# Optimization experiments

Hardware: AMD Instinct MI355X
Metric: run time of the kernel (lower is better)

Reference implementation:

```python
import jax, jax.numpy as jnp
import numpy as np

B, A, G = 16, 32, 512      # batch, atoms, g_feat_in
S, M = 1024, 8             # subset samples, peaks per subset
E, OH = 5, 20              # element types, thermometer size per element
FE = E * OH                # formula encoding = 100
D = 512                    # internal_d
NBINS = 512                # spect bins
EPS = 1e-4


def _ln(x, g, b):
    m = x.mean(-1, keepdims=True)
    v = jnp.mean((x - m) ** 2, -1, keepdims=True)
    return (x - m) * jax.lax.rsqrt(v + 1e-5) * g + b


def setup_inputs() -> dict:
    key = jax.random.key(0)
    ks = jax.random.split(key, 16)
    vert_feat_in = jax.random.normal(ks[0], (B, A, G), jnp.float32)
    vert_mask_in = jnp.ones((B, A), jnp.float32)
    elem = jax.random.randint(ks[1], (B, A), 0, E)
    vert_element_oh = jax.nn.one_hot(elem, E, dtype=jnp.float32)
    atom_subsets = jax.random.randint(ks[2], (B, S, A), 0, 2).astype(jnp.int32)
    atom_subsets_peaks_mass_idx = jax.random.randint(ks[3], (B, S, M), 0, NBINS).astype(jnp.int32)
    atom_subsets_peaks_intensity = jax.random.uniform(ks[4], (B, S, M), jnp.float32)

    def lin(k, o, i):
        s = 1.0 / np.sqrt(i)
        return jax.random.uniform(k, (o, i), jnp.float32, -s, s)

    return dict(
        vert_feat_in=vert_feat_in, vert_mask_in=vert_mask_in,
        vert_element_oh=vert_element_oh, atom_subsets=atom_subsets,
        atom_subsets_peaks_mass_idx=atom_subsets_peaks_mass_idx,
        atom_subsets_peaks_intensity=atom_subsets_peaks_intensity,
        ln_sub_g=jnp.ones((G,)), ln_sub_b=jnp.zeros((G,)),
        W_ih=lin(ks[5], 3 * G, FE), W_hh=lin(ks[6], 3 * G, G),
        b_ih=jnp.zeros((3 * G,)), b_hh=jnp.zeros((3 * G,)),
        ln_post_g=jnp.ones((G,)), ln_post_b=jnp.zeros((G,)),
        W1=lin(ks[7], D, G), b1=jnp.zeros((D,)),
        W2a=lin(ks[8], D, D), b2a=jnp.zeros((D,)),
        W2b=lin(ks[9], D, D), b2b=jnp.zeros((D,)),
        ln_pre_g=jnp.ones((D,)), ln_pre_b=jnp.zeros((D,)),
        W_s=lin(ks[10], 1, D), b_s=jnp.zeros((1,)),
    )


def reference(vert_feat_in, vert_mask_in, vert_element_oh, atom_subsets,
              atom_subsets_peaks_mass_idx, atom_subsets_peaks_intensity,
              ln_sub_g, ln_sub_b, W_ih, W_hh, b_ih, b_hh,
              ln_post_g, ln_post_b, W1, b1, W2a, b2a, W2b, b2b,
              ln_pre_g, ln_pre_b, W_s, b_s):
    subs_f = atom_subsets.astype(jnp.float32)
    masked_vert = vert_feat_in * vert_mask_in[:, :, None]          # B,A,G
    subs_masked = subs_f * vert_mask_in[:, None, :]                 # B,S,A
    # subset-weighted pooling of vertex features
    swv_sum = jnp.einsum('baf,bsa->bsf', masked_vert, subs_masked)  # B,S,G
    subset_size = subs_masked.sum(-1) + EPS                         # B,S
    swv_mean = swv_sum / subset_size[..., None]
    h = _ln(swv_mean, ln_sub_g, ln_sub_b)                           # B,S,G
    # formula counts -> thermometer (accumulating) one-hot; .byte() cast kills grads
    counts = jax.lax.stop_gradient(
        jnp.einsum('bae,bsa->bse', vert_element_oh, subs_f))        # B,S,E
    therm = (jnp.arange(OH, dtype=jnp.float32)[None, None, None, :] < counts[..., None])
    formulae = therm.astype(jnp.float32).reshape(counts.shape[0], counts.shape[1], FE)
    # GRUCell: input=formula encoding, hidden=subset_normed
    gi = jnp.einsum('bsf,gf->bsg', formulae, W_ih) + b_ih           # B,S,3G
    gh = jnp.einsum('bsh,gh->bsg', h, W_hh) + b_hh
    gi_r, gi_z, gi_n = jnp.split(gi, 3, axis=-1)
    gh_r, gh_z, gh_n = jnp.split(gh, 3, axis=-1)
    r = jax.nn.sigmoid(gi_r + gh_r)
    z = jax.nn.sigmoid(gi_z + gh_z)
    n = jnp.tanh(gi_n + r * gh_n)
    combined = (1.0 - z) * n + z * h                                # B,S,G
    x = _ln(combined, ln_post_g, ln_post_b)
    x = jax.nn.relu(jnp.einsum('bsg,dg->bsd', x, W1) + b1)
    x = jax.nn.relu(jnp.einsum('bsd,ed->bse', x, W2a) + b2a)
    x = jax.nn.relu(jnp.einsum('bsd,ed->bse', x, W2b) + b2b)
    x = _ln(x, ln_pre_g, ln_pre_b)
    scores = (jnp.einsum('bsd,od->bso', x, W_s) + b_s)[..., 0]      # B,S
    probs = jax.nn.softmax(scores, axis=-1)                         # B,S
    # sparse mass-matrix multiply: scatter subset probs into spectrum bins
    weighted = atom_subsets_peaks_intensity * probs[:, :, None]     # B,S,M
    bidx = jnp.arange(probs.shape[0])[:, None, None]
    spect_out = jnp.zeros((probs.shape[0], NBINS), probs.dtype)
    spect_out = spect_out.at[bidx, atom_subsets_peaks_mass_idx].add(weighted)
    return spect_out, probs
```

## Files before the change

kernel.cpp:

```cpp
#include <hip/hip_runtime.h>

#define NB 16
#define NA 32
#define NG 512
#define NS 1024
#define NM 8
#define NE 5
#define NOH 20
#define NFE 100
#define ND 512
#define NBINS 512
#define NTOK (NB * NS)

typedef unsigned short ushort_t;
typedef __attribute__((ext_vector_type(8))) short bf16x8;
typedef __attribute__((ext_vector_type(4))) float f32x4;

__device__ __forceinline__ ushort_t f2bf(float x) {
  union { float f; unsigned u; } v; v.f = x;
  unsigned r = v.u + 0x7FFF + ((v.u >> 16) & 1);
  return (ushort_t)(r >> 16);
}
__device__ __forceinline__ float bf2f(ushort_t b) {
  union { unsigned u; float f; } v; v.u = ((unsigned)b) << 16;
  return v.f;
}

__device__ __forceinline__ void gload_lds16(const void* g, void* l) {
  __builtin_amdgcn_global_load_lds(
      (const __attribute__((address_space(1))) void*)g,
      (__attribute__((address_space(3))) void*)l, 16, 0, 0);
}

__device__ __forceinline__ float wsum64(float v) {
#pragma unroll
  for (int off = 32; off > 0; off >>= 1) v += __shfl_xor(v, off);
  return v;
}

__device__ __forceinline__ float fsig(float x) {
  return __builtin_amdgcn_rcpf(1.f + __expf(-x));
}
__device__ __forceinline__ float ftanh(float x) {
  float t = fminf(fmaxf(x, -15.f), 15.f);
  return 1.f - 2.f * __builtin_amdgcn_rcpf(__expf(2.f * t) + 1.f);
}

__global__ __launch_bounds__(256) void setup_kernel(
    const float* __restrict__ vert, const float* __restrict__ mask,
    const float* __restrict__ eloh, const int* __restrict__ subs,
    const float* __restrict__ Wih, const float* __restrict__ bih,
    const float* __restrict__ Whh,
    const float* __restrict__ W1, const float* __restrict__ W2a,
    const float* __restrict__ W2b,
    float* __restrict__ tcd, ushort_t* __restrict__ PSb,
    ushort_t* __restrict__ o_hh, ushort_t* __restrict__ o1,
    ushort_t* __restrict__ o2a, ushort_t* __restrict__ o2b,
    ushort_t* __restrict__ VmT, ushort_t* __restrict__ S_bf) {
  int i = blockIdx.x * 256 + threadIdx.x;
  if (i < NTOK) {
    int b = i >> 10;
    const int* srow = subs + (size_t)i * NA;
    float cnt[NE] = {0.f, 0.f, 0.f, 0.f, 0.f};
    float z = 0.f;
    for (int a = 0; a < NA; a++) {
      float sb = (float)srow[a];
      z += sb * mask[b * NA + a];
      const float* eo = eloh + (size_t)(b * NA + a) * NE;
#pragma unroll
      for (int e = 0; e < NE; e++) cnt[e] += eo[e] * sb;
    }
    float* o = tcd + (size_t)i * 8;
#pragma unroll
    for (int e = 0; e < NE; e++) o[e] = cnt[e];
    o[5] = 1.0f / (z + 1e-4f);
    return;
  }
  i -= NTOK;
  if (i < NE * 1536) {
    int e = i / 1536, g = i % 1536;
    float s = (e == 0) ? bih[g] : 0.f;
    ushort_t* base = PSb + ((size_t)e * 21) * 1536 + g;
    base[0] = f2bf(s);
    for (int c = 1; c <= NOH; c++) {
      s += Wih[(size_t)g * NFE + e * NOH + (c - 1)];
      base[(size_t)c * 1536] = f2bf(s);
    }
    return;
  }
  i -= NE * 1536;
  if (i < 1536 * NG) { o_hh[i] = f2bf(Whh[i]); return; }
  i -= 1536 * NG;
  if (i < ND * NG) { o1[i] = f2bf(W1[i]); return; }
  i -= ND * NG;
  if (i < ND * ND) { o2a[i] = f2bf(W2a[i]); return; }
  i -= ND * ND;
  if (i < ND * ND) { o2b[i] = f2bf(W2b[i]); return; }
  i -= ND * ND;
  const int nV = NB * NG * NA;
  if (i < nV) {
    int b = i / (NG * NA); int rem = i % (NG * NA);
    int f = rem >> 5, a = rem & 31;
    float mk = mask[b * NA + a];
    VmT[i] = f2bf(vert[(size_t)b * NA * NG + a * NG + f] * mk * mk);
    return;
  }
  i -= nV;
  if (i < NTOK * NA) S_bf[i] = f2bf((float)subs[i]);
}

__global__ __launch_bounds__(256) void pool_gemm(
    const ushort_t* __restrict__ S_bf, const ushort_t* __restrict__ VmT,
    const float* __restrict__ tcd, float* __restrict__ SWV, int tok0) {
  __shared__ ushort_t As[128 * 32];
  __shared__ ushort_t Bs[128 * 32];
  const int t = threadIdx.x;
  const int w = t >> 6, lane = t & 63;
  const int wr = w >> 1, wc = w & 1;
  const int bm = blockIdx.x * 128;
  const int bn = blockIdx.y * 128;
  const int b = (tok0 + bm) >> 10;
  const int srow = lane >> 2;
  const int scol = (((lane & 3) ^ ((lane >> 3) & 3)) * 8);
  const ushort_t* Bbase = VmT + (size_t)b * NG * NA;
  gload_lds16(S_bf + (size_t)(tok0 + bm + w * 16 + srow) * 32 + scol, &As[w * 512]);
  gload_lds16(S_bf + (size_t)(tok0 + bm + 64 + w * 16 + srow) * 32 + scol, &As[2048 + w * 512]);
  gload_lds16(Bbase + (size_t)(bn + w * 16 + srow) * 32 + scol, &Bs[w * 512]);
  gload_lds16(Bbase + (size_t)(bn + 64 + w * 16 + srow) * 32 + scol, &Bs[2048 + w * 512]);
  __syncthreads();

  const int lr = lane & 15, lq = lane >> 4;
  const int rchunk = (lq ^ ((lr >> 1) & 3)) * 8;
  f32x4 acc[4][4];
#pragma unroll
  for (int m = 0; m < 4; m++)
#pragma unroll
    for (int n = 0; n < 4; n++) acc[m][n] = (f32x4)0.f;
  bf16x8 a[4], bb[4];
#pragma unroll
  for (int m = 0; m < 4; m++)
    a[m] = *(const bf16x8*)&As[(wr * 64 + m * 16 + lr) * 32 + rchunk];
#pragma unroll
  for (int n = 0; n < 4; n++)
    bb[n] = *(const bf16x8*)&Bs[(wc * 64 + n * 16 + lr) * 32 + rchunk];
#pragma unroll
  for (int m = 0; m < 4; m++)
#pragma unroll
    for (int n = 0; n < 4; n++)
      acc[m][n] = __builtin_amdgcn_mfma_f32_16x16x32_bf16(a[m], bb[n], acc[m][n], 0, 0, 0);

#pragma unroll
  for (int n = 0; n < 4; n++) {
    const int col = bn + wc * 64 + n * 16 + lr;
#pragma unroll
    for (int m = 0; m < 4; m++) {
      f32x4 v = acc[m][n];
#pragma unroll
      for (int r = 0; r < 4; r++) {
        int row = bm + wr * 64 + m * 16 + lq * 4 + r;
        float inv = tcd[(size_t)(tok0 + row) * 8 + 5];
        SWV[(size_t)row * NG + col] = v[r] * inv;
      }
    }
  }
}

__global__ __launch_bounds__(256) void finish_kernel(
    const float* __restrict__ SWV, const float* __restrict__ lng,
    const float* __restrict__ lnb, ushort_t* __restrict__ Hb) {
  const int t = threadIdx.x;
  const int lane = t & 63, wv = t >> 6;
  const int ltok = blockIdx.x * 4 + wv;
  const int f = lane * 8;
  const float* row = SWV + (size_t)ltok * NG + f;
  float4 v0 = *(const float4*)row;
  float4 v1 = *(const float4*)(row + 4);
  float x[8] = {v0.x, v0.y, v0.z, v0.w, v1.x, v1.y, v1.z, v1.w};
  float ps = 0.f;
#pragma unroll
  for (int j = 0; j < 8; j++) ps += x[j];
  float mean = wsum64(ps) * (1.0f / NG);
  float pq = 0.f;
#pragma unroll
  for (int j = 0; j < 8; j++) { float d = x[j] - mean; pq += d * d; }
  float rstd = rsqrtf(wsum64(pq) * (1.0f / NG) + 1e-5f);
  float4 g0 = *(const float4*)&lng[f], g1 = *(const float4*)&lng[f + 4];
  float4 b0 = *(const float4*)&lnb[f], b1 = *(const float4*)&lnb[f + 4];
  float gg[8] = {g0.x, g0.y, g0.z, g0.w, g1.x, g1.y, g1.z, g1.w};
  float bbv[8] = {b0.x, b0.y, b0.z, b0.w, b1.x, b1.y, b1.z, b1.w};
  bf16x8 ho;
#pragma unroll
  for (int j = 0; j < 8; j++) ho[j] = (short)f2bf((x[j] - mean) * rstd * gg[j] + bbv[j]);
  *(bf16x8*)&Hb[(size_t)ltok * NG + f] = ho;
}

__global__ __launch_bounds__(256) void gemm_bf16(
    const ushort_t* __restrict__ A, const ushort_t* __restrict__ W,
    const float* __restrict__ bias, ushort_t* __restrict__ C,
    int K, int Dout, int mode) {
  __shared__ ushort_t As[2][4096];
  __shared__ ushort_t Bs[2][4096];
  const int t = threadIdx.x;
  const int w = t >> 6;
  const int lane = t & 63;
  const int wr = w >> 1, wc = w & 1;
  const int bm = blockIdx.x * 128, bn = blockIdx.y * 128;

  const int srow = lane >> 2;
  const int scol = (((lane & 3) ^ ((lane >> 3) & 3)) * 8);
  const ushort_t* Ag0 = A + (size_t)(bm + w * 16 + srow) * K + scol;
  const ushort_t* Ag1 = A + (size_t)(bm + 64 + w * 16 + srow) * K + scol;
  const ushort_t* Wg0 = W + (size_t)(bn + w * 16 + srow) * K + scol;
  const ushort_t* Wg1 = W + (size_t)(bn + 64 + w * 16 + srow) * K + scol;
  const int l0 = w * 512;
  const int l1 = 2048 + w * 512;

  const int lr = lane & 15;
  const int lq = lane >> 4;
  const int rchunk = (lq ^ ((lr >> 1) & 3)) * 8;

  f32x4 acc[4][4];
#pragma unroll
  for (int m = 0; m < 4; m++)
#pragma unroll
    for (int n = 0; n < 4; n++) acc[m][n] = (f32x4)0.f;

  gload_lds16(Ag0, &As[0][l0]);
  gload_lds16(Ag1, &As[0][l1]);
  gload_lds16(Wg0, &Bs[0][l0]);
  gload_lds16(Wg1, &Bs[0][l1]);
  __syncthreads();

  const int nk = K >> 5;
  int cur = 0;
  for (int kt = 0; kt < nk; kt++) {
    if (kt + 1 < nk) {
      const int k1 = (kt + 1) << 5;
      gload_lds16(Ag0 + k1, &As[cur ^ 1][l0]);
      gload_lds16(Ag1 + k1, &As[cur ^ 1][l1]);
      gload_lds16(Wg0 + k1, &Bs[cur ^ 1][l0]);
      gload_lds16(Wg1 + k1, &Bs[cur ^ 1][l1]);
    }
    bf16x8 a[4], b[4];
#pragma unroll
    for (int m = 0; m < 4; m++)
      a[m] = *(const bf16x8*)&As[cur][(wr * 64 + m * 16 + lr) * 32 + rchunk];
#pragma unroll
    for (int n = 0; n < 4; n++)
      b[n] = *(const bf16x8*)&Bs[cur][(wc * 64 + n * 16 + lr) * 32 + rchunk];
#pragma unroll
    for (int m = 0; m < 4; m++)
#pragma unroll
      for (int n = 0; n < 4; n++)
        acc[m][n] = __builtin_amdgcn_mfma_f32_16x16x32_bf16(a[m], b[n], acc[m][n], 0, 0, 0);
    __syncthreads();
    cur ^= 1;
  }

  ushort_t* sc = (w < 2) ? &As[w][0] : &Bs[w - 2][0];
#pragma unroll
  for (int n = 0; n < 4; n++) {
    const float bv = bias[bn + wc * 64 + n * 16 + lr];
#pragma unroll
    for (int m = 0; m < 4; m++) {
      f32x4 v = acc[m][n];
#pragma unroll
      for (int r = 0; r < 4; r++) {
        const int row = m * 16 + lq * 4 + r;
        float u = v[r] + bv;
        if (mode == 1) u = fmaxf(u, 0.f);
        sc[row * 64 + ((n * 16 + lr) ^ ((row & 7) << 3))] = f2bf(u);
      }
    }
  }
  __builtin_amdgcn_s_waitcnt(0);
#pragma unroll
  for (int p = 0; p < 8; p++) {
    const int row = p * 8 + (lane >> 3);
    bf16x8 pk = *(const bf16x8*)&sc[row * 64 + (((lane & 7) * 8) ^ ((row & 7) << 3))];
    *(bf16x8*)&C[(size_t)(bm + wr * 64 + row) * Dout + bn + wc * 64 + (lane & 7) * 8] = pk;
  }
}

__global__ __launch_bounds__(256) void gate_ln_kernel(
    const ushort_t* __restrict__ Gh, const ushort_t* __restrict__ Hb,
    const float* __restrict__ tcd, const ushort_t* __restrict__ PSb,
    const float* __restrict__ lng, const float* __restrict__ lnb,
    ushort_t* __restrict__ X0) {
  const int t = threadIdx.x;
  const int lane = t & 63, wv = t >> 6;
  const int ltok = blockIdx.x * 4 + wv;
  const int f = lane * 8;
  int c[NE];
#pragma unroll
  for (int e = 0; e < NE; e++) {
    int ci = (int)tcd[(size_t)ltok * 8 + e];
    c[e] = ci > NOH ? NOH : ci;
  }
  float gir[8] = {0.f, 0.f, 0.f, 0.f, 0.f, 0.f, 0.f, 0.f};
  float giz[8] = {0.f, 0.f, 0.f, 0.f, 0.f, 0.f, 0.f, 0.f};
  float gin[8] = {0.f, 0.f, 0.f, 0.f, 0.f, 0.f, 0.f, 0.f};
#pragma unroll
  for (int e = 0; e < NE; e++) {
    const ushort_t* pe = PSb + ((size_t)(e * 21 + c[e])) * 1536;
    bf16x8 pr = *(const bf16x8*)&pe[f];
    bf16x8 pz = *(const bf16x8*)&pe[NG + f];
    bf16x8 pn = *(const bf16x8*)&pe[2 * NG + f];
#pragma unroll
    for (int j = 0; j < 8; j++) {
      gir[j] += bf2f((ushort_t)pr[j]);
      giz[j] += bf2f((ushort_t)pz[j]);
      gin[j] += bf2f((ushort_t)pn[j]);
    }
  }

  const ushort_t* gh = Gh + (size_t)ltok * 1536;
  bf16x8 vr = *(const bf16x8*)&gh[f];
  bf16x8 vz = *(const bf16x8*)&gh[NG + f];
  bf16x8 vn = *(const bf16x8*)&gh[2 * NG + f];
  bf16x8 vh = *(const bf16x8*)&Hb[(size_t)ltok * NG + f];
  float cv[8];
  float ps = 0.f;
#pragma unroll
  for (int j = 0; j < 8; j++) {
    float rg = fsig(gir[j] + bf2f((ushort_t)vr[j]));
    float zg = fsig(giz[j] + bf2f((ushort_t)vz[j]));
    float ng = ftanh(gin[j] + rg * bf2f((ushort_t)vn[j]));
    cv[j] = (1.f - zg) * ng + zg * bf2f((ushort_t)vh[j]);
    ps += cv[j];
  }
  float mean = wsum64(ps) * (1.0f / NG);
  float pq = 0.f;
#pragma unroll
  for (int j = 0; j < 8; j++) { float d = cv[j] - mean; pq += d * d; }
  float rstd = rsqrtf(wsum64(pq) * (1.0f / NG) + 1e-5f);
  float4 g0 = *(const float4*)&lng[f], g1 = *(const float4*)&lng[f + 4];
  float4 b0 = *(const float4*)&lnb[f], b1 = *(const float4*)&lnb[f + 4];
  float gg[8] = {g0.x, g0.y, g0.z, g0.w, g1.x, g1.y, g1.z, g1.w};
  float bbv[8] = {b0.x, b0.y, b0.z, b0.w, b1.x, b1.y, b1.z, b1.w};
  bf16x8 xo;
#pragma unroll
  for (int j = 0; j < 8; j++) xo[j] = (short)f2bf((cv[j] - mean) * rstd * gg[j] + bbv[j]);
  *(bf16x8*)&X0[(size_t)ltok * NG + f] = xo;
}

__global__ __launch_bounds__(256) void ln_score_kernel(
    const ushort_t* __restrict__ X, const float* __restrict__ lng,
    const float* __restrict__ lnb, const float* __restrict__ Wsc,
    const float* __restrict__ bsc, float* __restrict__ scores) {
  const int t = threadIdx.x;
  const int lane = t & 63, wv = t >> 6;
  const int ltok = blockIdx.x * 4 + wv;
  const int f = lane * 8;
  bf16x8 xx = *(const bf16x8*)&X[(size_t)ltok * ND + f];
  float x[8];
  float ps = 0.f;
#pragma unroll
  for (int j = 0; j < 8; j++) { x[j] = bf2f((ushort_t)xx[j]); ps += x[j]; }
  float mean = wsum64(ps) * (1.0f / ND);
  float pq = 0.f;
#pragma unroll
  for (int j = 0; j < 8; j++) { float d = x[j] - mean; pq += d * d; }
  float rstd = rsqrtf(wsum64(pq) * (1.0f / ND) + 1e-5f);
  float4 g0 = *(const float4*)&lng[f], g1 = *(const float4*)&lng[f + 4];
  float4 b0 = *(const float4*)&lnb[f], b1 = *(const float4*)&lnb[f + 4];
  float4 w0 = *(const float4*)&Wsc[f], w1 = *(const float4*)&Wsc[f + 4];
  float gg[8] = {g0.x, g0.y, g0.z, g0.w, g1.x, g1.y, g1.z, g1.w};
  float bbv[8] = {b0.x, b0.y, b0.z, b0.w, b1.x, b1.y, b1.z, b1.w};
  float ww[8] = {w0.x, w0.y, w0.z, w0.w, w1.x, w1.y, w1.z, w1.w};
  float d = 0.f;
#pragma unroll
  for (int j = 0; j < 8; j++) d += ((x[j] - mean) * rstd * gg[j] + bbv[j]) * ww[j];
  float dot = wsum64(d);
  if (lane == 0) scores[ltok] = dot + bsc[0];
}

__global__ __launch_bounds__(256) void softmax_scatter_kernel(
    const float* __restrict__ scores, const int* __restrict__ pidx,
    const float* __restrict__ pint, float* __restrict__ spect,
    float* __restrict__ probs) {
  const int b = blockIdx.x;
  const int t = threadIdx.x;
  __shared__ float s_red[4];
  __shared__ float s_spec[NBINS];
  const float* sc = scores + (size_t)b * NS;
  float v[4];
  float mx = -1e30f;
#pragma unroll
  for (int i = 0; i < 4; i++) { v[i] = sc[t + i * 256]; mx = fmaxf(mx, v[i]); }
#pragma unroll
  for (int off = 32; off > 0; off >>= 1) mx = fmaxf(mx, __shfl_down(mx, off));
  if ((t & 63) == 0) s_red[t >> 6] = mx;
  __syncthreads();
  mx = fmaxf(fmaxf(s_red[0], s_red[1]), fmaxf(s_red[2], s_red[3]));
  float e[4], sum = 0.f;
#pragma unroll
  for (int i = 0; i < 4; i++) { e[i] = expf(v[i] - mx); sum += e[i]; }
#pragma unroll
  for (int off = 32; off > 0; off >>= 1) sum += __shfl_down(sum, off);
  __syncthreads();
  if ((t & 63) == 0) s_red[t >> 6] = sum;
  __syncthreads();
  sum = s_red[0] + s_red[1] + s_red[2] + s_red[3];
  float inv = 1.f / sum;
  s_spec[t] = 0.f; s_spec[t + 256] = 0.f;
  float p[4];
#pragma unroll
  for (int i = 0; i < 4; i++) {
    p[i] = e[i] * inv;
    probs[(size_t)b * NS + t + i * 256] = p[i];
  }
  __syncthreads();
#pragma unroll
  for (int i = 0; i < 4; i++) {
    const int s = t + i * 256;
    const int* idx = pidx + ((size_t)b * NS + s) * NM;
    const float* wt = pint + ((size_t)b * NS + s) * NM;
#pragma unroll
    for (int m = 0; m < NM; m++)
      atomicAdd(&s_spec[idx[m]], wt[m] * p[i]);
  }
  __syncthreads();
  spect[(size_t)b * NBINS + t] = s_spec[t];
  spect[(size_t)b * NBINS + t + 256] = s_spec[t + 256];
}

extern "C" void kernel_launch(void* const* d_in, const int* in_sizes, int n_in,
                              void* d_out, int out_size, void* d_ws, size_t ws_size,
                              hipStream_t stream) {
  const float* vert = (const float*)d_in[0];
  const float* mask = (const float*)d_in[1];
  const float* eloh = (const float*)d_in[2];
  const int* subs = (const int*)d_in[3];
  const int* pidx = (const int*)d_in[4];
  const float* pint = (const float*)d_in[5];
  const float* ln_sub_g = (const float*)d_in[6];
  const float* ln_sub_b = (const float*)d_in[7];
  const float* W_ih = (const float*)d_in[8];
  const float* W_hh = (const float*)d_in[9];
  const float* b_ih = (const float*)d_in[10];
  const float* b_hh = (const float*)d_in[11];
  const float* ln_post_g = (const float*)d_in[12];
  const float* ln_post_b = (const float*)d_in[13];
  const float* W1 = (const float*)d_in[14];
  const float* b1 = (const float*)d_in[15];
  const float* W2a = (const float*)d_in[16];
  const float* b2a = (const float*)d_in[17];
  const float* W2b = (const float*)d_in[18];
  const float* b2b = (const float*)d_in[19];
  const float* ln_pre_g = (const float*)d_in[20];
  const float* ln_pre_b = (const float*)d_in[21];
  const float* W_s = (const float*)d_in[22];
  const float* b_s = (const float*)d_in[23];

  float* out = (float*)d_out;
  float* probs = out + NB * NBINS;

  char* ws = (char*)d_ws;
  float* scores = (float*)ws;
  ushort_t* Whh_bf = (ushort_t*)(ws + 65536);
  ushort_t* W1_bf  = (ushort_t*)(ws + 1638400);
  ushort_t* W2a_bf = (ushort_t*)(ws + 2162688);
  ushort_t* W2b_bf = (ushort_t*)(ws + 2686976);
  ushort_t* VmT    = (ushort_t*)(ws + 3211264);
  ushort_t* S_bf   = (ushort_t*)(ws + 3735552);
  float*    tcd    = (float*)(ws + 4784128);
  ushort_t* PSb    = (ushort_t*)(ws + 5308416);
  const size_t fixed = 5630976;

  const size_t per_tok = 7168;
  int T = NTOK;
  while (T > 1024 && fixed + (size_t)T * per_tok > ws_size) T >>= 1;
  const int nchunks = NTOK / T;

  char* cb = ws + fixed;
  float*    SWV = (float*)cb;                             cb += (size_t)T * 2048;
  ushort_t* Hb  = (ushort_t*)cb;                          cb += (size_t)T * 1024;
  ushort_t* Gh  = (ushort_t*)cb;                          cb += (size_t)T * 3072;
  ushort_t* X0  = (ushort_t*)cb;
  ushort_t* X1  = Gh;
  ushort_t* X2  = Gh + (size_t)T * 512;
  ushort_t* X3  = X0;

  const int setup_items = NTOK + NE * 1536 + 1536 * NG + ND * NG + 2 * ND * ND
                        + NB * NG * NA + NTOK * NA;
  setup_kernel<<<(setup_items + 255) / 256, 256, 0, stream>>>(
      vert, mask, eloh, subs, W_ih, b_ih, W_hh, W1, W2a, W2b,
      tcd, PSb, Whh_bf, W1_bf, W2a_bf, W2b_bf, VmT, S_bf);

  for (int c = 0; c < nchunks; c++) {
    const int tok0 = c * T;

    dim3 gp(T / 128, NG / 128);
    pool_gemm<<<gp, 256, 0, stream>>>(S_bf, VmT, tcd, SWV, tok0);
    finish_kernel<<<T / 4, 256, 0, stream>>>(SWV, ln_sub_g, ln_sub_b, Hb);

    dim3 g1(T / 128, 1536 / 128);
    gemm_bf16<<<g1, 256, 0, stream>>>(Hb, Whh_bf, b_hh, Gh, NG, 1536, 3);

    gate_ln_kernel<<<T / 4, 256, 0, stream>>>(Gh, Hb, tcd + (size_t)tok0 * 8, PSb,
                                              ln_post_g, ln_post_b, X0);

    dim3 g2(T / 128, ND / 128);
    gemm_bf16<<<g2, 256, 0, stream>>>(X0, W1_bf, b1, X1, NG, ND, 1);
    gemm_bf16<<<g2, 256, 0, stream>>>(X1, W2a_bf, b2a, X2, ND, ND, 1);
    gemm_bf16<<<g2, 256, 0, stream>>>(X2, W2b_bf, b2b, X3, ND, ND, 1);

    ln_score_kernel<<<T / 4, 256, 0, stream>>>(X3, ln_pre_g, ln_pre_b, W_s, b_s,
                                               scores + tok0);
  }

  softmax_scatter_kernel<<<NB, 256, 0, stream>>>(scores, pidx, pint, out, probs);
}
```

Baseline: 251.0 us.

## Fuse pooling GEMM with LayerNorm to drop fp32 intermediate buffer

Merges the pooling GEMM and the subsequent LayerNorm into one kernel. Each block now computes all 512 features for 32 tokens, reduces sum and sum of squares through shuffles and shared memory, and writes normalized bf16 directly. This removes the fp32 SWV round trip through global memory and one kernel launch. In exchange it uses the single-pass E[x^2]-mean^2 variance formula, which is less numerically stable, issues scalar 2-byte stores, and reloads the whole per-batch V slice in every block.

Result: faster. 241.9 us (-3.6%).

```diff
diff --git a/kernel.cpp b/kernel.cpp
--- a/kernel.cpp
+++ b/kernel.cpp
@@ -109,89 +109,99 @@
   if (i < NTOK * NA) S_bf[i] = f2bf((float)subs[i]);
 }
 
-__global__ __launch_bounds__(256) void pool_gemm(
+__global__ __launch_bounds__(256) void pool_ln_kernel(
     const ushort_t* __restrict__ S_bf, const ushort_t* __restrict__ VmT,
-    const float* __restrict__ tcd, float* __restrict__ SWV, int tok0) {
-  __shared__ ushort_t As[128 * 32];
-  __shared__ ushort_t Bs[128 * 32];
+    const float* __restrict__ tcd, const float* __restrict__ lng,
+    const float* __restrict__ lnb, ushort_t* __restrict__ Hb, int tok0) {
+  __shared__ ushort_t Sb[32 * 32];
+  __shared__ ushort_t Vb[512 * 32];
+  __shared__ float red_s[4][32];
+  __shared__ float red_q[4][32];
   const int t = threadIdx.x;
   const int w = t >> 6, lane = t & 63;
-  const int wr = w >> 1, wc = w & 1;
-  const int bm = blockIdx.x * 128;
-  const int bn = blockIdx.y * 128;
+  const int bm = blockIdx.x * 32;
   const int b = (tok0 + bm) >> 10;
+  const int scol = (((lane & 3) ^ ((lane >> 3) & 3)) * 8);
   const int srow = lane >> 2;
-  const int scol = (((lane & 3) ^ ((lane >> 3) & 3)) * 8);
-  const ushort_t* Bbase = VmT + (size_t)b * NG * NA;
-  gload_lds16(S_bf + (size_t)(tok0 + bm + w * 16 + srow) * 32 + scol, &As[w * 512]);
-  gload_lds16(S_bf + (size_t)(tok0 + bm + 64 + w * 16 + srow) * 32 + scol, &As[2048 + w * 512]);
-  gload_lds16(Bbase + (size_t)(bn + w * 16 + srow) * 32 + scol, &Bs[w * 512]);
-  gload_lds16(Bbase + (size_t)(bn + 64 + w * 16 + srow) * 32 + scol, &Bs[2048 + w * 512]);
+  if (w < 2)
+    gload_lds16(S_bf + (size_t)(tok0 + bm + w * 16 + srow) * 32 + scol, &Sb[(w * 16) * 32]);
+  const ushort_t* Vg = VmT + (size_t)b * NG * NA;
+#pragma unroll
+  for (int i = 0; i < 8; i++)
+    gload_lds16(Vg + (size_t)(i * 64 + w * 16 + srow) * 32 + scol, &Vb[(i * 64 + w * 16) * 32]);
   __syncthreads();
 
   const int lr = lane & 15, lq = lane >> 4;
   const int rchunk = (lq ^ ((lr >> 1) & 3)) * 8;
-  f32x4 acc[4][4];
-#pragma unroll
-  for (int m = 0; m < 4; m++)
-#pragma unroll
-    for (int n = 0; n < 4; n++) acc[m][n] = (f32x4)0.f;
-  bf16x8 a[4], bb[4];
-#pragma unroll
-  for (int m = 0; m < 4; m++)
-    a[m] = *(const bf16x8*)&As[(wr * 64 + m * 16 + lr) * 32 + rchunk];
-#pragma unroll
-  for (int n = 0; n < 4; n++)
-    bb[n] = *(const bf16x8*)&Bs[(wc * 64 + n * 16 + lr) * 32 + rchunk];
-#pragma unroll
-  for (int m = 0; m < 4; m++)
-#pragma unroll
-    for (int n = 0; n < 4; n++)
-      acc[m][n] = __builtin_amdgcn_mfma_f32_16x16x32_bf16(a[m], bb[n], acc[m][n], 0, 0, 0);
-
-#pragma unroll
-  for (int n = 0; n < 4; n++) {
-    const int col = bn + wc * 64 + n * 16 + lr;
-#pragma unroll
-    for (int m = 0; m < 4; m++) {
-      f32x4 v = acc[m][n];
+  bf16x8 a[2], bv[8];
+#pragma unroll
+  for (int m = 0; m < 2; m++)
+    a[m] = *(const bf16x8*)&Sb[(m * 16 + lr) * 32 + rchunk];
+#pragma unroll
+  for (int n = 0; n < 8; n++)
+    bv[n] = *(const bf16x8*)&Vb[(w * 128 + n * 16 + lr) * 32 + rchunk];
+  f32x4 acc[2][8];
+#pragma unroll
+  for (int m = 0; m < 2; m++)
+#pragma unroll
+    for (int n = 0; n < 8; n++) {
+      acc[m][n] = (f32x4)0.f;
+      acc[m][n] = __builtin_amdgcn_mfma_f32_16x16x32_bf16(a[m], bv[n], acc[m][n], 0, 0, 0);
+    }
+
+  float ps[2][4], pq[2][4];
+#pragma unroll
+  for (int m = 0; m < 2; m++)
+#pragma unroll
+    for (int r = 0; r < 4; r++) {
+      const int token = m * 16 + lq * 4 + r;
+      const float inv = tcd[(size_t)(tok0 + bm + token) * 8 + 5];
+      float s = 0.f, q = 0.f;
+#pragma unroll
+      for (int n = 0; n < 8; n++) {
+        float v = acc[m][n][r] * inv;
+        acc[m][n][r] = v;
+        s += v; q += v * v;
+      }
+      ps[m][r] = s; pq[m][r] = q;
+    }
+#pragma unroll
+  for (int off = 1; off < 16; off <<= 1) {
+#pragma unroll
+    for (int m = 0; m < 2; m++)
 #pragma unroll
       for (int r = 0; r < 4; r++) {
-        int row = bm + wr * 64 + m * 16 + lq * 4 + r;
-        float inv = tcd[(size_t)(tok0 + row) * 8 + 5];
-        SWV[(size_t)row * NG + col] = v[r] * inv;
+        ps[m][r] += __shfl_xor(ps[m][r], off);
+        pq[m][r] += __shfl_xor(pq[m][r], off);
       }
-    }
-  }
-}
-
-__global__ __launch_bounds__(256) void finish_kernel(
-    const float* __restrict__ SWV, const float* __restrict__ lng,
-    const float* __restrict__ lnb, ushort_t* __restrict__ Hb) {
-  const int t = threadIdx.x;
-  const int lane = t & 63, wv = t >> 6;
-  const int ltok = blockIdx.x * 4 + wv;
-  const int f = lane * 8;
-  const float* row = SWV + (size_t)ltok * NG + f;
-  float4 v0 = *(const float4*)row;
-  float4 v1 = *(const float4*)(row + 4);
-  float x[8] = {v0.x, v0.y, v0.z, v0.w, v1.x, v1.y, v1.z, v1.w};
-  float ps = 0.f;
-#pragma unroll
-  for (int j = 0; j < 8; j++) ps += x[j];
-  float mean = wsum64(ps) * (1.0f / NG);
-  float pq = 0.f;
-#pragma unroll
-  for (int j = 0; j < 8; j++) { float d = x[j] - mean; pq += d * d; }
-  float rstd = rsqrtf(wsum64(pq) * (1.0f / NG) + 1e-5f);
-  float4 g0 = *(const float4*)&lng[f], g1 = *(const float4*)&lng[f + 4];
-  float4 b0 = *(const float4*)&lnb[f], b1 = *(const float4*)&lnb[f + 4];
-  float gg[8] = {g0.x, g0.y, g0.z, g0.w, g1.x, g1.y, g1.z, g1.w};
-  float bbv[8] = {b0.x, b0.y, b0.z, b0.w, b1.x, b1.y, b1.z, b1.w};
-  bf16x8 ho;
-#pragma unroll
-  for (int j = 0; j < 8; j++) ho[j] = (short)f2bf((x[j] - mean) * rstd * gg[j] + bbv[j]);
-  *(bf16x8*)&Hb[(size_t)ltok * NG + f] = ho;
+  }
+  if (lr == 0) {
+#pragma unroll
+    for (int m = 0; m < 2; m++)
+#pragma unroll
+      for (int r = 0; r < 4; r++) {
+        red_s[w][m * 16 + lq * 4 + r] = ps[m][r];
+        red_q[w][m * 16 + lq * 4 + r] = pq[m][r];
+      }
+  }
+  __syncthreads();
+#pragma unroll
+  for (int m = 0; m < 2; m++)
+#pragma unroll
+    for (int r = 0; r < 4; r++) {
+      const int token = m * 16 + lq * 4 + r;
+      float tot = red_s[0][token] + red_s[1][token] + red_s[2][token] + red_s[3][token];
+      float totq = red_q[0][token] + red_q[1][token] + red_q[2][token] + red_q[3][token];
+      float mean = tot * (1.0f / NG);
+      float var = totq * (1.0f / NG) - mean * mean;
+      float rstd = rsqrtf(var + 1e-5f);
+      ushort_t* hrow = Hb + (size_t)(bm + token) * NG;
+#pragma unroll
+      for (int n = 0; n < 8; n++) {
+        const int f = w * 128 + n * 16 + lr;
+        hrow[f] = f2bf((acc[m][n][r] - mean) * rstd * lng[f] + lnb[f]);
+      }
+    }
 }
 
 __global__ __launch_bounds__(256) void gemm_bf16(
@@ -468,13 +478,12 @@
   ushort_t* PSb    = (ushort_t*)(ws + 5308416);
   const size_t fixed = 5630976;
 
-  const size_t per_tok = 7168;
+  const size_t per_tok = 5120;
   int T = NTOK;
   while (T > 1024 && fixed + (size_t)T * per_tok > ws_size) T >>= 1;
   const int nchunks = NTOK / T;
 
   char* cb = ws + fixed;
-  float*    SWV = (float*)cb;                             cb += (size_t)T * 2048;
   ushort_t* Hb  = (ushort_t*)cb;                          cb += (size_t)T * 1024;
   ushort_t* Gh  = (ushort_t*)cb;                          cb += (size_t)T * 3072;
   ushort_t* X0  = (ushort_t*)cb;
@@ -491,9 +500,8 @@
   for (int c = 0; c < nchunks; c++) {
     const int tok0 = c * T;
 
-    dim3 gp(T / 128, NG / 128);
-    pool_gemm<<<gp, 256, 0, stream>>>(S_bf, VmT, tcd, SWV, tok0);
-    finish_kernel<<<T / 4, 256, 0, stream>>>(SWV, ln_sub_g, ln_sub_b, Hb);
+    pool_ln_kernel<<<T / 32, 256, 0, stream>>>(S_bf, VmT, tcd, ln_sub_g, ln_sub_b,
+                                               Hb, tok0);
 
     dim3 g1(T / 128, 1536 / 128);
     gemm_bf16<<<g1, 256, 0, stream>>>(Hb, Whh_bf, b_hh, Gh, NG, 1536, 3);
```
